# Kernel tuning notes

Measured on AMD Instinct MI355X. Metric: run time of the kernel, lower is better.

The kernel has to match this reference:

```python
import jax, jax.numpy as jnp
import numpy as np

B, N, FN, FE, H, FC, OUT = 64, 32, 32, 16, 32, 128, 1
ENN_LAYERS, S2S_STEPS = 3, 3


def setup_inputs() -> dict:
    key = jax.random.key(0)
    ks = jax.random.split(key, 16)
    s = 0.1
    return {
        "x": jax.random.uniform(ks[0], (B, N, FN), dtype=jnp.float32),
        "edge": jax.random.normal(ks[1], (B, N, N, FE), dtype=jnp.float32),
        "adjacency": jax.random.randint(ks[2], (B, N, N), 0, 2).astype(jnp.float32),
        # embedding layer
        "W_emb": s * jax.random.normal(ks[3], (FN, H)),
        "b_emb": jnp.zeros((H,), jnp.float32),
        # edge MLP: FE -> FC -> H*H
        "W1": s * jax.random.normal(ks[4], (FE, FC)),
        "b1": jnp.zeros((FC,), jnp.float32),
        "W2": s * jax.random.normal(ks[5], (FC, H * H)),
        "b2": jnp.zeros((H * H,), jnp.float32),
        # GRU (torch layout: weight_ih [3H,H], weight_hh [3H,H])
        "gru_Wi": s * jax.random.normal(ks[6], (3 * H, H)),
        "gru_Wh": s * jax.random.normal(ks[7], (3 * H, H)),
        "gru_bi": jnp.zeros((3 * H,), jnp.float32),
        "gru_bh": jnp.zeros((3 * H,), jnp.float32),
        # Set2Set LSTM: input 2H, hidden H (torch layout weight_ih [4H,2H])
        "lstm_Wi": s * jax.random.normal(ks[8], (4 * H, 2 * H)),
        "lstm_Wh": s * jax.random.normal(ks[9], (4 * H, H)),
        "lstm_bi": jnp.zeros((4 * H,), jnp.float32),
        "lstm_bh": jnp.zeros((4 * H,), jnp.float32),
        # output fc: 2H -> OUT
        "Wf": s * jax.random.normal(ks[10], (2 * H, OUT)),
        "bf": jnp.zeros((OUT,), jnp.float32),
    }


def reference(x, edge, adjacency, W_emb, b_emb, W1, b1, W2, b2,
              gru_Wi, gru_Wh, gru_bi, gru_bh,
              lstm_Wi, lstm_Wh, lstm_bi, lstm_bh, Wf, bf):
    Bx, Nx, _ = x.shape
    Hd = W_emb.shape[1]
    # node mask: (sum over raw features > 0), [B,N,1]
    msk = (jnp.sum(x, axis=2, keepdims=True) > 0).astype(x.dtype)
    h = x @ W_emb + b_emb  # [B,N,H]
    # per-edge weight matrices from edge MLP (same every layer in the original)
    ew = (jax.nn.relu(edge @ W1 + b1) @ W2 + b2).reshape(Bx, Nx, Nx, Hd, Hd)
    for _ in range(ENN_LAYERS):
        # msg[b,i,j,:] = ew[b,i,j] @ h[b,i]; masked by adjacency, summed over source i
        m = jnp.einsum('bijuv,biv->biju', ew, h) * adjacency[..., None]
        m = m.sum(axis=1)  # [B,N,H]
        # single-step GRU (torch gate order r,z,n)
        gi = m @ gru_Wi.T + gru_bi
        gh = h @ gru_Wh.T + gru_bh
        ir, iz, inn = jnp.split(gi, 3, axis=-1)
        hr, hz, hn = jnp.split(gh, 3, axis=-1)
        r = jax.nn.sigmoid(ir + hr)
        z = jax.nn.sigmoid(iz + hz)
        n = jnp.tanh(inn + r * hn)
        h = msk * ((1.0 - z) * n + z * h)
    # Set2Set readout (single-layer LSTM, torch gate order i,f,g,o)
    q = jnp.zeros((Bx, Hd), x.dtype)
    c = jnp.zeros((Bx, Hd), x.dtype)
    q_star = jnp.zeros((Bx, 2 * Hd), x.dtype)
    for _ in range(S2S_STEPS):
        g = q_star @ lstm_Wi.T + lstm_bi + q @ lstm_Wh.T + lstm_bh
        gi_, gf_, gg_, go_ = jnp.split(g, 4, axis=-1)
        c = jax.nn.sigmoid(gf_) * c + jax.nn.sigmoid(gi_) * jnp.tanh(gg_)
        q = jax.nn.sigmoid(go_) * jnp.tanh(c)
        e = jnp.einsum('bnh,bh->bn', h, q)
        e = jnp.where(msk[..., 0] == 0, -jnp.inf, e)
        a = jax.nn.softmax(e, axis=1)
        r = jnp.sum(a[..., None] * h * msk, axis=1)
        q_star = jnp.concatenate([q, r], axis=-1)
    return q_star @ Wf + bf  # [B,OUT]
```

## Files before the change

kernel.cpp:

```cpp
#include <hip/hip_runtime.h>
#include <hip/hip_bf16.h>
#include <math.h>

typedef __attribute__((ext_vector_type(8))) short bf16x8;
typedef __attribute__((ext_vector_type(16))) float f32x16;

__device__ __forceinline__ float sigf(float x) { return 1.0f / (1.0f + expf(-x)); }

__global__ __launch_bounds__(256, 4) void k_prep(
    const float* __restrict__ edge, const float* __restrict__ adj,
    const float* __restrict__ W1, const float* __restrict__ b1,
    const float* __restrict__ x, const float* __restrict__ W_emb,
    const float* __restrict__ b_emb, const float* __restrict__ W2,
    const float* __restrict__ gWi, const float* __restrict__ gWh,
    const float* __restrict__ b2, const float* __restrict__ lWi,
    const float* __restrict__ lWh,
    __hip_bfloat16* __restrict__ taT2, __hip_bfloat16* __restrict__ W2FTB,
    float* __restrict__ h, float* __restrict__ msk,
    float* __restrict__ gWiT, float* __restrict__ gWhT, float* __restrict__ b2T,
    float* __restrict__ lWiT, float* __restrict__ lWhT) {
    __shared__ float es[512];
    __shared__ float adjv[32];
    __shared__ float xs[256];
    __shared__ short t_lds[4096];
    const int tid = threadIdx.x, bid = blockIdx.x;
    const int b = bid >> 5, j = bid & 31;
    const int c = tid & 127, g = tid >> 7;
    float wr[16];
    #pragma unroll
    for (int v = 0; v < 16; ++v) wr[v] = W1[v * 128 + c];
    const float b1c = b1[c];
    if (tid < 128) {
        int i = tid >> 2, k4 = tid & 3;
        ((float4*)es)[tid] = *(const float4*)&edge[(((long)(b * 32 + i)) * 32 + j) * 16 + k4 * 4];
    } else if (tid < 160) {
        int i = tid - 128;
        adjv[i] = adj[(b * 32 + i) * 32 + j];
    }
    if (bid < 256) xs[tid] = x[bid * 256 + tid];
    __syncthreads();
    {
        #pragma unroll
        for (int ii = 0; ii < 16; ++ii) {
            int i = g * 16 + ii;
            const float* er = es + i * 16;
            float acc = b1c;
            #pragma unroll
            for (int k = 0; k < 16; ++k) acc += er[k] * wr[k];
            float val = adjv[i] * fmaxf(acc, 0.f);
            t_lds[c * 32 + i] = (short)__bfloat16_as_ushort(__float2bfloat16(val));
        }
    }
    __syncthreads();
    {
        int4* dst = (int4*)(taT2 + (long)bid * 4096);
        const int4* src = (const int4*)t_lds;
        dst[tid] = src[tid];
        dst[tid + 256] = src[tid + 256];
    }
    if (bid < 256) {
        int r = tid >> 5, u = tid & 31;
        int rowe = bid * 8 + r;
        float acc = b_emb[u];
        #pragma unroll
        for (int k = 0; k < 32; ++k) acc += xs[r * 32 + k] * W_emb[k * 32 + u];
        h[rowe * 32 + u] = acc;
        if (u == 0) {
            float s = 0.f;
            #pragma unroll
            for (int k = 0; k < 32; ++k) s += xs[r * 32 + k];
            msk[rowe] = (s > 0.f) ? 1.f : 0.f;
        }
    } else if (bid < 384) {
        int base = (bid - 256) * 1024;
        #pragma unroll
        for (int q = 0; q < 4; ++q) {
            int idx = base + q * 256 + tid;
            int chunk = idx >> 9, u = (idx >> 4) & 31, inner = idx & 15;
            int cv = chunk * 16 + inner;
            int cc = cv >> 5, v = cv & 31;
            W2FTB[idx] = __float2bfloat16(W2[cc * 1024 + u * 32 + v]);
        }
    } else if (bid == 384) {
        for (int idx = tid; idx < 3072; idx += 256) gWiT[(idx & 31) * 96 + (idx >> 5)] = gWi[idx];
        for (int idx = tid; idx < 3072; idx += 256) gWhT[(idx & 31) * 96 + (idx >> 5)] = gWh[idx];
        for (int idx = tid; idx < 1024; idx += 256) b2T[(idx & 31) * 32 + (idx >> 5)] = b2[idx];
        for (int idx = tid; idx < 8192; idx += 256) lWiT[(idx & 63) * 128 + (idx >> 6)] = lWi[idx];
        for (int idx = tid; idx < 4096; idx += 256) lWhT[(idx & 31) * 128 + (idx >> 5)] = lWh[idx];
    }
}

__global__ __launch_bounds__(256, 2) void k_msg(
    const __hip_bfloat16* __restrict__ taT2, const __hip_bfloat16* __restrict__ W2FTB,
    const float* __restrict__ h, float* __restrict__ partial) {
    __shared__ __align__(16) char P_lds[65536];
    __shared__ __align__(16) short hT[1024];
    const int tid = threadIdx.x, bid = blockIdx.x;
    const int b = bid >> 2, cq = bid & 3;
    const int w = tid >> 6, l = tid & 63, lid = l & 31, kh = l >> 5;
    for (int idx = tid; idx < 1024; idx += 256)
        hT[(idx & 31) * 32 + (idx >> 5)] =
            (short)__bfloat16_as_ushort(__float2bfloat16(h[b * 1024 + idx]));
    __syncthreads();
    const short* taB = (const short*)taT2 + (long)b * 131072;
    const short* w2b = (const short*)W2FTB;
    const short* hTp = hT + lid * 32 + kh * 8;
    bf16x8 hb0 = *(const bf16x8*)hTp;
    bf16x8 hb1 = *(const bf16x8*)(hTp + 16);
    #pragma unroll 2
    for (int q = 0; q < 8; ++q) {
        int jj = w * 8 + q;
        const short* ap = taB + (jj * 128 + cq * 32 + lid) * 32 + kh * 8;
        bf16x8 a0 = *(const bf16x8*)ap;
        bf16x8 a1 = *(const bf16x8*)(ap + 16);
        f32x16 accg = {};
        accg = __builtin_amdgcn_mfma_f32_32x32x16_bf16(a0, hb0, accg, 0, 0, 0);
        accg = __builtin_amdgcn_mfma_f32_32x32x16_bf16(a1, hb1, accg, 0, 0, 0);
        #pragma unroll
        for (int r = 0; r < 16; ++r) {
            int crow = (r & 3) + 8 * (r >> 2) + 4 * kh;
            int byte = (crow * 2 + (lid >> 4)) * 1024 + ((lid >> 3) & 1) * 512
                     + jj * 16 + (lid & 7) * 2;
            *(short*)(P_lds + byte) =
                (short)__bfloat16_as_ushort(__float2bfloat16(accg[r]));
        }
    }
    __syncthreads();
    f32x16 acc = {};
    #pragma unroll
    for (int kk = 0; kk < 16; ++kk) {
        int slice = w * 16 + kk;
        bf16x8 a = *(const bf16x8*)(P_lds + slice * 1024 + kh * 512 + lid * 16);
        bf16x8 bg = *(const bf16x8*)(w2b + (cq * 64 + slice) * 512 + lid * 16 + kh * 8);
        acc = __builtin_amdgcn_mfma_f32_32x32x16_bf16(a, bg, acc, 0, 0, 0);
    }
    __syncthreads();
    {
        float* red = (float*)P_lds + w * 1024;
        #pragma unroll
        for (int r = 0; r < 16; ++r) {
            int crow = (r & 3) + 8 * (r >> 2) + 4 * kh;
            red[crow * 32 + lid] = acc[r];
        }
    }
    __syncthreads();
    {
        float* r0 = (float*)P_lds;
        for (int k = tid; k < 1024; k += 256)
            partial[(long)bid * 1024 + k] = r0[k] + r0[1024 + k] + r0[2048 + k] + r0[3072 + k];
    }
}

__global__ __launch_bounds__(256, 2) void k_gru(
    const float* __restrict__ partial, const float* __restrict__ h,
    const float* __restrict__ adj, const float* __restrict__ msk,
    const float* __restrict__ b2T, const float* __restrict__ gWiT,
    const float* __restrict__ gWhT, const float* __restrict__ gbi,
    const float* __restrict__ gbh, float* __restrict__ hout) {
    __shared__ float hsh[1024], adjs[1024], wWiT[3072], wWhT[3072], b2s[1024];
    __shared__ float hsumL[256], mLs[256], gbs[192];
    const int tid = threadIdx.x, bid = blockIdx.x;
    const int b = bid >> 2, jc = bid & 3;
    const int j8 = tid >> 5, u = tid & 31, jg = jc * 8 + j8;
    for (int k = tid; k < 1024; k += 256) hsh[k] = h[b * 1024 + k];
    for (int k = tid; k < 1024; k += 256) adjs[k] = adj[b * 1024 + k];
    for (int k = tid; k < 3072; k += 256) wWiT[k] = gWiT[k];
    for (int k = tid; k < 3072; k += 256) wWhT[k] = gWhT[k];
    for (int k = tid; k < 1024; k += 256) b2s[k] = b2T[k];
    if (tid < 96) gbs[tid] = gbi[tid];
    else if (tid < 192) gbs[tid] = gbh[tid - 96];
    float ps = 0.f;
    #pragma unroll
    for (int cq = 0; cq < 4; ++cq)
        ps += partial[((long)(b * 4 + cq)) * 1024 + jc * 256 + tid];
    __syncthreads();
    float hs = 0.f;
    #pragma unroll
    for (int i = 0; i < 32; ++i) hs += adjs[i * 32 + jg] * hsh[i * 32 + u];
    hsumL[tid] = hs;
    __syncthreads();
    float m = ps;
    #pragma unroll
    for (int v = 0; v < 32; ++v) m += b2s[v * 32 + u] * hsumL[j8 * 32 + v];
    mLs[tid] = m;
    __syncthreads();
    float gi[3], gh[3];
    #pragma unroll
    for (int kb = 0; kb < 3; ++kb) {
        int k = kb * 32 + u;
        float a = gbs[k], c = gbs[96 + k];
        #pragma unroll
        for (int v = 0; v < 32; ++v) {
            a += mLs[j8 * 32 + v] * wWiT[v * 96 + k];
            c += hsh[jg * 32 + v] * wWhT[v * 96 + k];
        }
        gi[kb] = a; gh[kb] = c;
    }
    float r = sigf(gi[0] + gh[0]);
    float z = sigf(gi[1] + gh[1]);
    float n = tanhf(gi[2] + r * gh[2]);
    float hv = hsh[jg * 32 + u];
    float mm = msk[b * 32 + jg];
    float res = mm * ((1.f - z) * n + z * hv);
    hout[b * 1024 + jg * 32 + u] = res;
}

__global__ __launch_bounds__(128, 4) void k_s2s(
    const float* __restrict__ h, const float* __restrict__ msk,
    const float* __restrict__ lWiT, const float* __restrict__ lWhT,
    const float* __restrict__ lbi, const float* __restrict__ lbh,
    const float* __restrict__ Wf, const float* __restrict__ bf,
    float* __restrict__ out) {
    __shared__ float hsh[1024];
    __shared__ float mskk[32], qs[32], cs2[32], qstar[64], gsv[128], asv[32];
    const int tid = threadIdx.x, b = blockIdx.x;
    for (int k = tid; k < 1024; k += 128) hsh[k] = h[b * 1024 + k];
    if (tid < 32) { mskk[tid] = msk[b * 32 + tid]; qs[tid] = 0.f; cs2[tid] = 0.f; }
    if (tid < 64) qstar[tid] = 0.f;
    __syncthreads();
    for (int step = 0; step < 3; ++step) {
        {
            float g = lbi[tid] + lbh[tid];
            #pragma unroll
            for (int pp = 0; pp < 64; ++pp) g += qstar[pp] * lWiT[pp * 128 + tid];
            #pragma unroll
            for (int v = 0; v < 32; ++v) g += qs[v] * lWhT[v * 128 + tid];
            gsv[tid] = g;
        }
        __syncthreads();
        if (tid < 32) {
            float ci = sigf(gsv[32 + tid]) * cs2[tid] + sigf(gsv[tid]) * tanhf(gsv[64 + tid]);
            cs2[tid] = ci;
            qs[tid] = sigf(gsv[96 + tid]) * tanhf(ci);
        }
        __syncthreads();
        if (tid < 32) {
            float e = 0.f;
            #pragma unroll
            for (int v = 0; v < 32; ++v) e += hsh[tid * 32 + v] * qs[v];
            e = (mskk[tid] == 0.f) ? -INFINITY : e;
            float mx = e;
            for (int o = 16; o >= 1; o >>= 1) mx = fmaxf(mx, __shfl_xor(mx, o, 64));
            float a = expf(e - mx);
            float ss = a;
            for (int o = 16; o >= 1; o >>= 1) ss += __shfl_xor(ss, o, 64);
            asv[tid] = a / ss;
        }
        __syncthreads();
        if (tid < 32) {
            float rr = 0.f;
            #pragma unroll
            for (int nn = 0; nn < 32; ++nn) rr += asv[nn] * hsh[nn * 32 + tid] * mskk[nn];
            qstar[tid] = qs[tid];
            qstar[32 + tid] = rr;
        }
        __syncthreads();
    }
    if (tid < 64) {
        float v = qstar[tid] * Wf[tid];
        for (int o = 32; o >= 1; o >>= 1) v += __shfl_xor(v, o, 64);
        if (tid == 0) out[b] = v + bf[0];
    }
}

extern "C" void kernel_launch(void* const* d_in, const int* in_sizes, int n_in,
                              void* d_out, int out_size, void* d_ws, size_t ws_size,
                              hipStream_t stream) {
    const float* x    = (const float*)d_in[0];
    const float* edge = (const float*)d_in[1];
    const float* adj  = (const float*)d_in[2];
    const float* W_emb= (const float*)d_in[3];
    const float* b_emb= (const float*)d_in[4];
    const float* W1   = (const float*)d_in[5];
    const float* b1   = (const float*)d_in[6];
    const float* W2   = (const float*)d_in[7];
    const float* b2   = (const float*)d_in[8];
    const float* gWi  = (const float*)d_in[9];
    const float* gWh  = (const float*)d_in[10];
    const float* gbi  = (const float*)d_in[11];
    const float* gbh  = (const float*)d_in[12];
    const float* lWi  = (const float*)d_in[13];
    const float* lWh  = (const float*)d_in[14];
    const float* lbi  = (const float*)d_in[15];
    const float* lbh  = (const float*)d_in[16];
    const float* Wf   = (const float*)d_in[17];
    const float* bf   = (const float*)d_in[18];
    float* out = (float*)d_out;

    __hip_bfloat16* taT2  = (__hip_bfloat16*)d_ws;
    __hip_bfloat16* W2FTB = taT2 + 8388608;
    float* hA   = (float*)(W2FTB + 131072);
    float* hB   = hA + 65536;
    float* mskp = hB + 65536;
    float* partial = mskp + 2048;
    float* gWiT = partial + 262144;
    float* gWhT = gWiT + 3072;
    float* b2T  = gWhT + 3072;
    float* lWiT = b2T + 1024;
    float* lWhT = lWiT + 8192;

    k_prep<<<2048, 256, 0, stream>>>(edge, adj, W1, b1, x, W_emb, b_emb, W2,
                                     gWi, gWh, b2, lWi, lWh,
                                     taT2, W2FTB, hA, mskp,
                                     gWiT, gWhT, b2T, lWiT, lWhT);
    float* hcur = hA; float* hnxt = hB;
    for (int l = 0; l < 3; ++l) {
        k_msg<<<256, 256, 0, stream>>>(taT2, W2FTB, hcur, partial);
        k_gru<<<256, 256, 0, stream>>>(partial, hcur, adj, mskp, b2T,
                                       gWiT, gWhT, gbi, gbh, hnxt);
        float* tf = hcur; hcur = hnxt; hnxt = tf;
    }
    k_s2s<<<64, 128, 0, stream>>>(hcur, mskp, lWiT, lWhT, lbi, lbh, Wf, bf, out);
}
```

Before: 101.8 us.

## Fuse GRU update into next message kernel and swizzle LDS staging

The GRU step for layer l is folded into the prologue of the layer l+1 message kernel. Each of the four column-quarter blocks per batch redundantly recomputes the full GRU for its batch, which removes two kernel launches and the round trip of h through global memory. Partial buffers are double-buffered to avoid read/write hazards across the fused launches. An XOR swizzle is also added to the P_lds write and read addresses to reduce LDS bank conflicts, at the cost of 4x redundant GRU arithmetic per batch.

Result: slower. 251.9 us (+147.3%).

```diff
diff --git a/kernel.cpp b/kernel.cpp
--- a/kernel.cpp
+++ b/kernel.cpp
@@ -6,6 +6,7 @@
 typedef __attribute__((ext_vector_type(16))) float f32x16;
 
 __device__ __forceinline__ float sigf(float x) { return 1.0f / (1.0f + expf(-x)); }
+__device__ __forceinline__ int swz(int b) { return b ^ ((b >> 5) & 0x30) ^ ((b >> 7) & 0x40); }
 
 __global__ __launch_bounds__(256, 4) void k_prep(
     const float* __restrict__ edge, const float* __restrict__ adj,
@@ -92,16 +93,101 @@
 
 __global__ __launch_bounds__(256, 2) void k_msg(
     const __hip_bfloat16* __restrict__ taT2, const __hip_bfloat16* __restrict__ W2FTB,
-    const float* __restrict__ h, float* __restrict__ partial) {
+    const float* __restrict__ hin, const float* __restrict__ partial_in,
+    float* __restrict__ hout,
+    const float* __restrict__ adj, const float* __restrict__ msk,
+    const float* __restrict__ b2T, const float* __restrict__ gWiT,
+    const float* __restrict__ gWhT, const float* __restrict__ gbi,
+    const float* __restrict__ gbh,
+    float* __restrict__ partial_out, int fuse) {
     __shared__ __align__(16) char P_lds[65536];
     __shared__ __align__(16) short hT[1024];
+    __shared__ float gbs[192], mskk[32];
     const int tid = threadIdx.x, bid = blockIdx.x;
     const int b = bid >> 2, cq = bid & 3;
     const int w = tid >> 6, l = tid & 63, lid = l & 31, kh = l >> 5;
-    for (int idx = tid; idx < 1024; idx += 256)
-        hT[(idx & 31) * 32 + (idx >> 5)] =
-            (short)__bfloat16_as_ushort(__float2bfloat16(h[b * 1024 + idx]));
-    __syncthreads();
+
+    if (!fuse) {
+        for (int idx = tid; idx < 1024; idx += 256)
+            hT[(idx & 31) * 32 + (idx >> 5)] =
+                (short)__bfloat16_as_ushort(__float2bfloat16(hin[b * 1024 + idx]));
+    } else {
+        float* hsh   = (float*)P_lds;
+        float* adjs  = hsh + 1024;
+        float* wWiT  = adjs + 1024;
+        float* wWhT  = wWiT + 3072;
+        float* b2s   = wWhT + 3072;
+        float* hsumL = b2s + 1024;
+        float* mLs   = hsumL + 1024;
+        for (int k = tid; k < 1024; k += 256) {
+            hsh[k] = hin[b * 1024 + k];
+            adjs[k] = adj[b * 1024 + k];
+            b2s[k] = b2T[k];
+        }
+        for (int k = tid; k < 3072; k += 256) { wWiT[k] = gWiT[k]; wWhT[k] = gWhT[k]; }
+        if (tid < 96) gbs[tid] = gbi[tid];
+        else if (tid < 192) gbs[tid] = gbh[tid - 96];
+        if (tid < 32) mskk[tid] = msk[b * 32 + tid];
+        float ps[4];
+        #pragma unroll
+        for (int p = 0; p < 4; ++p) {
+            float s = 0.f;
+            #pragma unroll
+            for (int cqq = 0; cqq < 4; ++cqq)
+                s += partial_in[((long)(b * 4 + cqq)) * 1024 + p * 256 + tid];
+            ps[p] = s;
+        }
+        __syncthreads();
+        const int j8 = tid >> 5, u = tid & 31;
+        #pragma unroll
+        for (int p = 0; p < 4; ++p) {
+            int j = j8 + p * 8;
+            float hs = 0.f;
+            #pragma unroll
+            for (int i = 0; i < 32; ++i) hs += adjs[i * 32 + j] * hsh[i * 32 + u];
+            hsumL[j * 32 + u] = hs;
+        }
+        __syncthreads();
+        #pragma unroll
+        for (int p = 0; p < 4; ++p) {
+            int j = j8 + p * 8;
+            float m = ps[p];
+            #pragma unroll
+            for (int v = 0; v < 32; ++v) m += b2s[v * 32 + u] * hsumL[j * 32 + v];
+            mLs[j * 32 + u] = m;
+        }
+        __syncthreads();
+        float res[4];
+        #pragma unroll
+        for (int p = 0; p < 4; ++p) {
+            int j = j8 + p * 8;
+            float gi[3], gh[3];
+            #pragma unroll
+            for (int kb = 0; kb < 3; ++kb) {
+                int k = kb * 32 + u;
+                float a = gbs[k], cgh = gbs[96 + k];
+                #pragma unroll
+                for (int v = 0; v < 32; ++v) {
+                    a   += mLs[j * 32 + v] * wWiT[v * 96 + k];
+                    cgh += hsh[j * 32 + v] * wWhT[v * 96 + k];
+                }
+                gi[kb] = a; gh[kb] = cgh;
+            }
+            float r = sigf(gi[0] + gh[0]);
+            float z = sigf(gi[1] + gh[1]);
+            float n = tanhf(gi[2] + r * gh[2]);
+            float hv = hsh[j * 32 + u];
+            res[p] = mskk[j] * ((1.f - z) * n + z * hv);
+        }
+        #pragma unroll
+        for (int p = 0; p < 4; ++p) {
+            int j = j8 + p * 8;
+            hT[u * 32 + j] = (short)__bfloat16_as_ushort(__float2bfloat16(res[p]));
+            if (cq == 0) hout[b * 1024 + j * 32 + u] = res[p];
+        }
+    }
+    __syncthreads();
+
     const short* taB = (const short*)taT2 + (long)b * 131072;
     const short* w2b = (const short*)W2FTB;
     const short* hTp = hT + lid * 32 + kh * 8;
@@ -110,7 +196,7 @@
     #pragma unroll 2
     for (int q = 0; q < 8; ++q) {
         int jj = w * 8 + q;
-        const short* ap = taB + (jj * 128 + cq * 32 + lid) * 32 + kh * 8;
+        const short* ap = taB + ((jj * 128 + cq * 32 + lid) * 32 + kh * 8);
         bf16x8 a0 = *(const bf16x8*)ap;
         bf16x8 a1 = *(const bf16x8*)(ap + 16);
         f32x16 accg = {};
@@ -121,7 +207,7 @@
             int crow = (r & 3) + 8 * (r >> 2) + 4 * kh;
             int byte = (crow * 2 + (lid >> 4)) * 1024 + ((lid >> 3) & 1) * 512
                      + jj * 16 + (lid & 7) * 2;
-            *(short*)(P_lds + byte) =
+            *(short*)(P_lds + swz(byte)) =
                 (short)__bfloat16_as_ushort(__float2bfloat16(accg[r]));
         }
     }
@@ -130,7 +216,7 @@
     #pragma unroll
     for (int kk = 0; kk < 16; ++kk) {
         int slice = w * 16 + kk;
-        bf16x8 a = *(const bf16x8*)(P_lds + slice * 1024 + kh * 512 + lid * 16);
+        bf16x8 a = *(const bf16x8*)(P_lds + swz(slice * 1024 + kh * 512 + lid * 16));
         bf16x8 bg = *(const bf16x8*)(w2b + (cq * 64 + slice) * 512 + lid * 16 + kh * 8);
         acc = __builtin_amdgcn_mfma_f32_32x32x16_bf16(a, bg, acc, 0, 0, 0);
     }
@@ -147,7 +233,7 @@
     {
         float* r0 = (float*)P_lds;
         for (int k = tid; k < 1024; k += 256)
-            partial[(long)bid * 1024 + k] = r0[k] + r0[1024 + k] + r0[2048 + k] + r0[3072 + k];
+            partial_out[(long)bid * 1024 + k] = r0[k] + r0[1024 + k] + r0[2048 + k] + r0[3072 + k];
     }
 }
 
@@ -201,8 +287,7 @@
     float n = tanhf(gi[2] + r * gh[2]);
     float hv = hsh[jg * 32 + u];
     float mm = msk[b * 32 + jg];
-    float res = mm * ((1.f - z) * n + z * hv);
-    hout[b * 1024 + jg * 32 + u] = res;
+    hout[b * 1024 + jg * 32 + u] = mm * ((1.f - z) * n + z * hv);
 }
 
 __global__ __launch_bounds__(128, 4) void k_s2s(
@@ -289,11 +374,14 @@
 
     __hip_bfloat16* taT2  = (__hip_bfloat16*)d_ws;
     __hip_bfloat16* W2FTB = taT2 + 8388608;
-    float* hA   = (float*)(W2FTB + 131072);
-    float* hB   = hA + 65536;
-    float* mskp = hB + 65536;
-    float* partial = mskp + 2048;
-    float* gWiT = partial + 262144;
+    float* h0   = (float*)(W2FTB + 131072);
+    float* h1   = h0 + 65536;
+    float* h2   = h1 + 65536;
+    float* h3   = h2 + 65536;
+    float* mskp = h3 + 65536;
+    float* partialA = mskp + 2048;
+    float* partialB = partialA + 262144;
+    float* gWiT = partialB + 262144;
     float* gWhT = gWiT + 3072;
     float* b2T  = gWhT + 3072;
     float* lWiT = b2T + 1024;
@@ -301,14 +389,18 @@
 
     k_prep<<<2048, 256, 0, stream>>>(edge, adj, W1, b1, x, W_emb, b_emb, W2,
                                      gWi, gWh, b2, lWi, lWh,
-                                     taT2, W2FTB, hA, mskp,
+                                     taT2, W2FTB, h0, mskp,
                                      gWiT, gWhT, b2T, lWiT, lWhT);
-    float* hcur = hA; float* hnxt = hB;
-    for (int l = 0; l < 3; ++l) {
-        k_msg<<<256, 256, 0, stream>>>(taT2, W2FTB, hcur, partial);
-        k_gru<<<256, 256, 0, stream>>>(partial, hcur, adj, mskp, b2T,
-                                       gWiT, gWhT, gbi, gbh, hnxt);
-        float* tf = hcur; hcur = hnxt; hnxt = tf;
-    }
-    k_s2s<<<64, 128, 0, stream>>>(hcur, mskp, lWiT, lWhT, lbi, lbh, Wf, bf, out);
+    k_msg<<<256, 256, 0, stream>>>(taT2, W2FTB, h0, nullptr, nullptr,
+                                   adj, mskp, b2T, gWiT, gWhT, gbi, gbh,
+                                   partialA, 0);
+    k_msg<<<256, 256, 0, stream>>>(taT2, W2FTB, h0, partialA, h1,
+                                   adj, mskp, b2T, gWiT, gWhT, gbi, gbh,
+                                   partialB, 1);
+    k_msg<<<256, 256, 0, stream>>>(taT2, W2FTB, h1, partialB, h2,
+                                   adj, mskp, b2T, gWiT, gWhT, gbi, gbh,
+                                   partialA, 1);
+    k_gru<<<256, 256, 0, stream>>>(partialA, h2, adj, mskp, b2T,
+                                   gWiT, gWhT, gbi, gbh, h3);
+    k_s2s<<<64, 128, 0, stream>>>(h3, mskp, lWiT, lWhT, lbi, lbh, Wf, bf, out);
 }
```
